# Kernel optimization log

Measured on AMD Instinct MI355X. Metric: run time of the kernel, lower is better.

Reference implementation:

```python
import jax, jax.numpy as jnp
from jax import lax
import numpy as np

D = 512        # d_model
F = 128        # raw feature dim
MS = 1024      # logic (service) nodes
NP_ = 16384    # physical nodes
EL = 4096      # logic edges
EP = 131072    # phys edges
SRC = 0        # source_node_idx
NEG = -1e9


def _gnn(feats, edge_index, Win, Wout, N):
    row, col = edge_index
    h = jax.nn.relu(feats @ Win)                                  # [N, D]
    agg = jax.ops.segment_sum(h[row], col, num_segments=N)        # [N, D]
    return jax.nn.relu((h + agg) @ Wout)


def _bfs_hop(edge_index, N, src, iters=16):
    # BFS hop distance from src (bounded Bellman-Ford relaxation)
    row, col = edge_index
    big = jnp.int32(N)
    dist = jnp.full((N,), big, jnp.int32).at[src].set(0)
    def body(_, d):
        cand = jnp.minimum(d[row] + 1, big)
        upd = jax.ops.segment_min(cand, col, num_segments=N)
        return jnp.minimum(d, upd)
    return lax.fori_loop(0, iters, body, dist)


def _forward(logic_feats, phys_feats, Ws_in, Ws_out, Wp_in, Wp_out,
             sA1, sA2, pA1, pA2, Wq, Wk, Wc1, bc1, wc2,
             logic_edge_index, phys_edge_index, actions, static_mask, topo_order):
    Np = phys_feats.shape[0]
    cloud = Np - 1                                                # cloud_node_idx = -1
    h_s = _gnn(logic_feats, logic_edge_index, Ws_in, Ws_out, logic_feats.shape[0])
    h_p = _gnn(phys_feats, phys_edge_index, Wp_in, Wp_out, Np)
    # task-specific residual adapters
    h_s = h_s + jax.nn.relu(h_s @ sA1) @ sA2
    h_p = h_p + jax.nn.relu(h_p @ pA1) @ pA2
    metric = _bfs_hop(phys_edge_index, Np, SRC)                   # [Np] int32
    q_all = (h_s @ Wq) / jnp.sqrt(jnp.float32(D))                 # [Ms, D]
    K = h_p @ Wk                                                  # [Np, D]
    acts = actions.astype(jnp.int32)

    def step(state, i):
        visited, last, logp_sum, ent_sum, switches, relax = state
        base = static_mask[i]                                     # [Np] bool
        # cloud_sticky branch
        sticky = jnp.zeros_like(base).at[cloud].set(base[cloud])
        # forbid_return (allow_stay keeps `last`)
        forbid = visited.at[last].set(False)
        allowed_n = base & (~forbid) & (metric >= metric[last])   # metric_non_decreasing
        allowed = jnp.where(last == cloud, sticky, allowed_n)
        any_a = allowed.any()
        # relaxation fallback: stay -> cloud -> base
        fb_stay = jnp.zeros_like(base).at[last].set(True)
        fb_cloud = jnp.zeros_like(base).at[cloud].set(True)
        fallback = jnp.where(base[last], fb_stay, jnp.where(base[cloud], fb_cloud, base))
        allowed = jnp.where(any_a, allowed, fallback)
        # actor: masked categorical over physical nodes
        logits = K @ q_all[i]                                     # [Np]
        logp_all = jax.nn.log_softmax(jnp.where(allowed, logits, NEG))
        p = jnp.exp(logp_all)
        ent = -jnp.sum(p * logp_all)
        a = acts[i]
        ne = a != last
        visited = visited.at[last].set(visited[last] | ne)
        last = jnp.where(ne, a, last)
        return (visited, last, logp_sum + logp_all[a], ent_sum + ent,
                switches + ne.astype(jnp.int32), relax + (~any_a).astype(jnp.int32)), None

    init = (jnp.zeros((Np,), bool), jnp.int32(SRC),
            jnp.float32(0.0), jnp.float32(0.0), jnp.int32(0), jnp.int32(0))
    (visited, last, logp_sum, ent_sum, switches, relax), _ = lax.scan(
        step, init, topo_order.astype(jnp.int32))
    # value head
    pooled = jnp.concatenate([h_s.mean(0), h_p.mean(0)])          # [2D]
    value = jax.nn.relu(pooled @ Wc1 + bc1) @ wc2                 # scalar
    return jnp.stack([logp_sum, ent_sum, value])


def setup_inputs() -> dict:
    key = jax.random.key(0)
    ks = jax.random.split(key, 20)
    s = 0.05
    def w(k, shape):
        return jax.random.normal(k, shape, jnp.float32) * s
    return {
        "logic_edge_index": jax.random.randint(ks[0], (2, EL), 0, MS, jnp.int32),
        "logic_feats": jax.random.normal(ks[1], (MS, F), jnp.float32),
        "phys_edge_index": jax.random.randint(ks[2], (2, EP), 0, NP_, jnp.int32),
        "phys_feats": jax.random.normal(ks[3], (NP_, F), jnp.float32),
        "actions": jax.random.randint(ks[4], (MS,), 0, NP_, jnp.int32),
        "static_mask": jnp.ones((MS, NP_), bool),
        "topo_order": jnp.arange(MS, dtype=jnp.int32),
        "Ws_in": w(ks[5], (F, D)), "Ws_out": w(ks[6], (D, D)),
        "Wp_in": w(ks[7], (F, D)), "Wp_out": w(ks[8], (D, D)),
        "sA1": w(ks[9], (D, D)), "sA2": w(ks[10], (D, D)),
        "pA1": w(ks[11], (D, D)), "pA2": w(ks[12], (D, D)),
        "Wq": w(ks[13], (D, D)), "Wk": w(ks[14], (D, D)),
        "Wc1": w(ks[15], (2 * D, D)),
        "bc1": jnp.zeros((D,), jnp.float32),
        "wc2": w(ks[16], (D,)),
    }


def reference(logic_edge_index, logic_feats, phys_edge_index, phys_feats,
              actions, static_mask, topo_order,
              Ws_in, Ws_out, Wp_in, Wp_out, sA1, sA2, pA1, pA2,
              Wq, Wk, Wc1, bc1, wc2):
    return _forward(logic_feats, phys_feats, Ws_in, Ws_out, Wp_in, Wp_out,
                    sA1, sA2, pA1, pA2, Wq, Wk, Wc1, bc1, wc2,
                    logic_edge_index, phys_edge_index, actions, static_mask, topo_order)
```

## Files before the change

### kernel.cpp

```cpp
#include <hip/hip_runtime.h>
#include <cstdint>
#include <cstddef>

typedef __bf16 bf16_t;
typedef bf16_t bf16x8 __attribute__((ext_vector_type(8)));
typedef bf16_t bf16x4v __attribute__((ext_vector_type(4)));
typedef float f32x4 __attribute__((ext_vector_type(4)));

#define NEGV (-1e9f)

#define GLDS(gp, lp) __builtin_amdgcn_global_load_lds( \
    (const __attribute__((address_space(1))) void*)(gp), \
    (__attribute__((address_space(3))) void*)(lp), 16, 0, 0)

struct PrepArgs {
    const float* w512src[8]; bf16_t* w512dst[8];
    const float* w128src[2]; bf16_t* w128dst[2];
    const float* logicF; const float* physF;
    bf16_t* featsSb; bf16_t* featsPb;
    const int* mask; uint32_t* bits;
    int* cntC; int* cntR; int* cntL; int* firstL; int* dist;
    float* pooled; float* hacc;
};

__global__ __launch_bounds__(256)
void k_prep(PrepArgs p) {
    __shared__ float tb[64][65];
    const int b = blockIdx.x, tid = threadIdx.x;
    if (b < 544) {
        const float* src; bf16_t* dst; int K, tile;
        if (b < 512) { src = p.w512src[b >> 6]; dst = p.w512dst[b >> 6]; K = 512; tile = b & 63; }
        else { int bb = b - 512; src = p.w128src[bb >> 4]; dst = p.w128dst[bb >> 4]; K = 128; tile = bb & 15; }
        const int N = 512;
        int kt = tile >> 3, tc = tile & 7;
        int cx = tid & 63, ry = tid >> 6;
#pragma unroll
        for (int q = 0; q < 16; ++q) {
            int r = q * 4 + ry;
            tb[r][cx] = src[(size_t)(kt * 64 + r) * N + tc * 64 + cx];
        }
        __syncthreads();
#pragma unroll
        for (int q = 0; q < 16; ++q) {
            int r2 = q * 4 + ry;
            dst[(size_t)(tc * 64 + r2) * K + kt * 64 + cx] = (bf16_t)tb[cx][r2];
        }
    } else if (b < 672) {
        size_t e0 = (size_t)(b - 544) * 1024 + tid * 4;
        float4 v = *(const float4*)(p.logicF + e0);
        bf16x4v o; o[0]=(bf16_t)v.x; o[1]=(bf16_t)v.y; o[2]=(bf16_t)v.z; o[3]=(bf16_t)v.w;
        *(bf16x4v*)(p.featsSb + e0) = o;
    } else if (b < 2720) {
        size_t e0 = (size_t)(b - 672) * 1024 + tid * 4;
        float4 v = *(const float4*)(p.physF + e0);
        bf16x4v o; o[0]=(bf16_t)v.x; o[1]=(bf16_t)v.y; o[2]=(bf16_t)v.z; o[3]=(bf16_t)v.w;
        *(bf16x4v*)(p.featsPb + e0) = o;
    } else if (b < 2784) {
        int gid = (b - 2720) * 256 + tid;
        p.cntC[gid] = 0; p.cntR[gid] = 0; p.firstL[gid] = 0x7fffffff;
        p.dist[gid] = (gid == 0) ? 0 : 16384;
        if (gid < 1024) { p.cntL[gid] = 0; p.pooled[gid] = 0.0f; }
        if (gid < 512) p.hacc[gid] = 0.0f;
    } else {
        size_t w = (size_t)(b - 2784) * 256 + tid;
        const int4* q4 = (const int4*)(p.mask + w * 32);
        uint32_t bb = 0;
#pragma unroll
        for (int q = 0; q < 8; ++q) {
            int4 v = q4[q];
            bb |= (v.x != 0 ? 1u : 0u) << (q * 4);
            bb |= (v.y != 0 ? 1u : 0u) << (q * 4 + 1);
            bb |= (v.z != 0 ? 1u : 0u) << (q * 4 + 2);
            bb |= (v.w != 0 ? 1u : 0u) << (q * 4 + 3);
        }
        p.bits[w] = bb;
    }
}

__global__ void k_hist3(const int* __restrict__ rowP, const int* __restrict__ colP,
                        const int* __restrict__ rowL, const int* __restrict__ colL,
                        int* cntC, int* cntR, int* cntL, int EP, int EL,
                        const int* __restrict__ topo, const int* __restrict__ acts,
                        int* __restrict__ lastArr, int* __restrict__ firstL) {
    int b = blockIdx.x;
    if (b < 1040) {
        int e = b * 256 + threadIdx.x;
        if (e < EP) atomicAdd(&cntC[colP[e]], 1);
        else if (e < 2 * EP) atomicAdd(&cntR[rowP[e - EP]], 1);
        else if (e < 2 * EP + EL) atomicAdd(&cntL[colL[e - 2 * EP]], 1);
    } else {
        int s = (b - 1040) * 256 + threadIdx.x;
        int last = (s == 0) ? 0 : acts[topo[s - 1]];
        lastArr[s] = last;
        int a = acts[topo[s]];
        if (a != last) atomicMin(&firstL[last], s);
    }
}

__global__ __launch_bounds__(256)
void k_scan3(int* cntC, int* offC, int* curC,
             int* cntR, int* offR, int* curR,
             int* cntL, int* offL, int* curL) {
    __shared__ int ss[256];
    int tid = threadIdx.x;
    const int* cnt; int* off; int* cur; int n;
    if (blockIdx.x == 0)      { cnt = cntC; off = offC; cur = curC; n = 16384; }
    else if (blockIdx.x == 1) { cnt = cntR; off = offR; cur = curR; n = 16384; }
    else                      { cnt = cntL; off = offL; cur = curL; n = 1024; }
    int chunk = n / 256, base = tid * chunk, s = 0;
    for (int i = 0; i < chunk; ++i) s += cnt[base + i];
    ss[tid] = s; __syncthreads();
    for (int d = 1; d < 256; d <<= 1) {
        int v = (tid >= d) ? ss[tid - d] : 0;
        __syncthreads(); ss[tid] += v; __syncthreads();
    }
    int run = (tid == 0) ? 0 : ss[tid - 1];
    for (int i = 0; i < chunk; ++i) { off[base + i] = run; cur[base + i] = run; run += cnt[base + i]; }
    if (tid == 255) off[n] = run;
}

__global__ void k_scatter3(const int* __restrict__ rowP, const int* __restrict__ colP,
                           const int* __restrict__ rowL, const int* __restrict__ colL,
                           int* curC, int* curR, int* curL,
                           int* erowCP, int* ecolRP, int* erowL, int EP, int EL) {
    int e = blockIdx.x * 256 + threadIdx.x;
    if (e < EP) {
        int c = colP[e]; int q = atomicAdd(&curC[c], 1); erowCP[q] = rowP[e];
    } else if (e < 2 * EP) {
        int e2 = e - EP;
        int c = rowP[e2]; int q = atomicAdd(&curR[c], 1); ecolRP[q] = colP[e2];
    } else if (e < 2 * EP + EL) {
        int e3 = e - 2 * EP;
        int c = colL[e3]; int q = atomicAdd(&curL[c], 1); erowL[q] = rowL[e3];
    }
}

__global__ __launch_bounds__(256)
void k_bfs_level(const int* __restrict__ offR, const int* __restrict__ ecol,
                 int* __restrict__ dist, int lev) {
    int j = blockIdx.x * 256 + threadIdx.x;
    if (dist[j] != lev) return;
    int e0 = offR[j], e1 = offR[j + 1];
    for (int e = e0; e < e1; ++e) {
        int v = ecol[e];
        if (dist[v] == 16384) dist[v] = lev + 1;
    }
}

__global__ __launch_bounds__(256)
void k_fmpack(const int* __restrict__ firstL, const int* __restrict__ dist, int* __restrict__ fm) {
    int j = blockIdx.x * 256 + threadIdx.x;
    int fl = firstL[j]; if (fl > 0xFFFF) fl = 0xFFFF;
    fm[j] = (fl << 16) | dist[j];
}

struct GemmDesc { const bf16_t* A; const bf16_t* B; const bf16_t* Cin; bf16_t* O;
                  int N; int K; float scale; int relu; };
struct GemmPair { GemmDesc d0; GemmDesc d1; int split; };

__global__ __launch_bounds__(256)
void gemm_mfma(GemmPair args) {
    __shared__ bf16_t As[2][128 * 32];
    __shared__ bf16_t Bs[2][128 * 32];
    const int nwg = gridDim.x * gridDim.y;
    const int cpx = nwg >> 3;
    const int pfl = blockIdx.y * gridDim.x + blockIdx.x;
    const int vfl = (pfl & 7) * cpx + (pfl >> 3);
    const int vbx = vfl % gridDim.x;
    const int vby = vfl / gridDim.x;
    const int inSet1 = (vby >= args.split);
    const GemmDesc g = inSet1 ? args.d1 : args.d0;
    const int my = vby - (inSet1 ? args.split : 0);
    const int m0 = my * 128, n0 = vbx * 128;
    const int tid = threadIdx.x, wave = tid >> 6, lane = tid & 63;
    const int wm = (wave >> 1) * 64, wn = (wave & 1) * 64;
    const int lr = lane & 15, lk = (lane >> 4) * 8;
    const int K = g.K;
    const int srr = wave * 16 + (lane >> 2);
    const int scb = (((lane & 3) ^ ((lane >> 2) & 3)) << 4);
    const char* Abase = (const char*)g.A + ((size_t)(m0 + srr) * K) * 2 + scb;
    const char* Bbase = (const char*)g.B + ((size_t)(n0 + srr) * K) * 2 + scb;
    const size_t rstep = (size_t)64 * K * 2;
    f32x4 acc[4][4] = {};

    auto stage = [&](int q, int k0) {
        const char* a0 = Abase + (size_t)k0 * 2;
        const char* b0 = Bbase + (size_t)k0 * 2;
        GLDS(a0,         &As[q][(wave * 16) * 32]);
        GLDS(a0 + rstep, &As[q][(64 + wave * 16) * 32]);
        GLDS(b0,         &Bs[q][(wave * 16) * 32]);
        GLDS(b0 + rstep, &Bs[q][(64 + wave * 16) * 32]);
    };

    stage(0, 0);
    asm volatile("s_waitcnt vmcnt(0)" ::: "memory");
    __syncthreads();
    const int nt = K >> 5;
    for (int t = 0; t < nt; ++t) {
        int cur = t & 1;
        if (t + 1 < nt) stage(cur ^ 1, (t + 1) << 5);
        bf16x8 af[4], bff[4];
#pragma unroll
        for (int mi = 0; mi < 4; ++mi) {
            int r = wm + mi * 16 + lr;
            int pb = r * 64 + ((lk * 2) ^ ((r & 3) << 4));
            af[mi] = *(const bf16x8*)((const char*)&As[cur][0] + pb);
        }
#pragma unroll
        for (int ni = 0; ni < 4; ++ni) {
            int r = wn + ni * 16 + lr;
            int pb = r * 64 + ((lk * 2) ^ ((r & 3) << 4));
            bff[ni] = *(const bf16x8*)((const char*)&Bs[cur][0] + pb);
        }
#pragma unroll
        for (int mi = 0; mi < 4; ++mi)
#pragma unroll
            for (int ni = 0; ni < 4; ++ni)
                acc[mi][ni] = __builtin_amdgcn_mfma_f32_16x16x32_bf16(af[mi], bff[ni], acc[mi][ni], 0, 0, 0);
        asm volatile("s_waitcnt vmcnt(0)" ::: "memory");
        __syncthreads();
    }
    const int rb = m0 + wm + (lane >> 4) * 4;
    const int cb = n0 + wn + lr;
#pragma unroll
    for (int mi = 0; mi < 4; ++mi)
#pragma unroll
        for (int ni = 0; ni < 4; ++ni)
#pragma unroll
            for (int r = 0; r < 4; ++r) {
                int row = rb + mi * 16 + r;
                int col = cb + ni * 16;
                size_t idx = (size_t)row * g.N + col;
                float v = acc[mi][ni][r] * g.scale;
                if (g.Cin) v += (float)g.Cin[idx];
                if (g.relu) v = fmaxf(v, 0.0f);
                g.O[idx] = (bf16_t)v;
            }
}

__global__ __launch_bounds__(256)
void k_spmm2(const bf16_t* __restrict__ HL, const int* __restrict__ offL, const int* __restrict__ erowL, bf16_t* __restrict__ XL,
             const bf16_t* __restrict__ HP, const int* __restrict__ offP, const int* __restrict__ erowP, bf16_t* __restrict__ XP) {
    int b = blockIdx.x;
    const bf16_t* H; const int* off; const int* erow; bf16_t* X; int c;
    int wib = threadIdx.x >> 6, lane = threadIdx.x & 63;
    if (b < 256) { H = HL; off = offL; erow = erowL; X = XL; c = b * 4 + wib; }
    else { b -= 256; H = HP; off = offP; erow = erowP; X = XP; c = b * 4 + wib; }
    int d0 = lane * 8;
    float acc[8] = {0,0,0,0,0,0,0,0};
    int e0 = off[c], e1 = off[c + 1];
    for (int e = e0; e < e1; ++e) {
        int r = erow[e];
        bf16x8 h = *(const bf16x8*)(H + (size_t)r * 512 + d0);
#pragma unroll
        for (int j = 0; j < 8; ++j) acc[j] += (float)h[j];
    }
    bf16x8 own = *(const bf16x8*)(H + (size_t)c * 512 + d0);
    bf16x8 o;
#pragma unroll
    for (int j = 0; j < 8; ++j) o[j] = (bf16_t)((float)own[j] + acc[j]);
    *(bf16x8*)(X + (size_t)c * 512 + d0) = o;
}

__global__ __launch_bounds__(256)
void k_scan2(const bf16_t* __restrict__ S, const uint32_t* __restrict__ bits,
             const int* __restrict__ fm, const int* __restrict__ topo,
             const int* __restrict__ acts, const int* __restrict__ lastA,
             float* __restrict__ slogp, float* __restrict__ sent) {
    const int NPn = 16384, cloud = NPn - 1;
    __shared__ float msh[256], zsh[256], wsh[256];
    __shared__ int ash[256];
    const int s = blockIdx.x, tid = threadIdx.x;
    const int i = topo[s], a = acts[i], last = lastA[s];
    const bf16_t* Srow = S + (size_t)i * NPn;
    const uint32_t* brow = bits + (size_t)i * 512;
    const int ml = fm[last] & 0xFFFF;
    const int baseCloud = (brow[511] >> 31) & 1;
    const int lic = (last == cloud);
    if (lic && baseCloud) {
        if (tid == 0) {
            float M = (float)Srow[cloud];
            slogp[s] = (a == cloud) ? 0.0f : (NEGV - M);
            sent[s] = 0.0f;
        }
        return;
    }
    float m = -3.4e38f, Z = 0.0f, W = 0.0f;
    int any = 0;
    if (!lic) {
        for (int c = 0; c < 8; ++c) {
            int j0 = c * 2048 + tid * 8;
            bf16x8 sv = *(const bf16x8*)(Srow + j0);
            uint32_t b8 = (brow[j0 >> 5] >> (j0 & 24)) & 0xFFu;
            int4 f0 = *(const int4*)(fm + j0);
            int4 f1 = *(const int4*)(fm + j0 + 4);
            int fj[8] = {f0.x, f0.y, f0.z, f0.w, f1.x, f1.y, f1.z, f1.w};
#pragma unroll
            for (int q = 0; q < 8; ++q) {
                int j = j0 + q;
                bool alw = ((b8 >> q) & 1) && ((fj[q] & 0xFFFF) >= ml)
                           && (j == last || (((unsigned)fj[q]) >> 16) >= (unsigned)s);
                if (alw) {
                    any = 1;
                    float l = (float)sv[q];
                    if (l > m) {
                        float d = m - l, ce = expf(d);
                        W = ce * (W + d * Z);
                        Z = ce * Z + 1.0f;
                        m = l;
                    } else {
                        float t = l - m, e = expf(t);
                        Z += e; W += t * e;
                    }
                }
            }
        }
    }
    msh[tid] = m; zsh[tid] = Z; wsh[tid] = W; ash[tid] = any;
    __syncthreads();
    for (int st = 128; st > 0; st >>= 1) {
        if (tid < st) {
            float m1 = msh[tid], Z1 = zsh[tid], W1 = wsh[tid];
            float m2 = msh[tid + st], Z2 = zsh[tid + st], W2 = wsh[tid + st];
            float M2 = fmaxf(m1, m2);
            float e1 = expf(m1 - M2), e2 = expf(m2 - M2);
            zsh[tid] = e1 * Z1 + e2 * Z2;
            wsh[tid] = e1 * (W1 + (m1 - M2) * Z1) + e2 * (W2 + (m2 - M2) * Z2);
            msh[tid] = M2;
            ash[tid] |= ash[tid + st];
        }
        __syncthreads();
    }
    if (tid != 0) return;
    if (ash[0]) {
        float M = msh[0], Zt = zsh[0], Wt = wsh[0];
        float logZ = logf(Zt);
        int fa = fm[a];
        bool alwa = ((brow[a >> 5] >> (a & 31)) & 1) && ((fa & 0xFFFF) >= ml)
                    && (a == last || (((unsigned)fa) >> 16) >= (unsigned)s);
        float la = alwa ? (float)Srow[a] : NEGV;
        slogp[s] = la - M - logZ;
        sent[s] = logZ - Wt / Zt;
        return;
    }
    int baseLast = (brow[last >> 5] >> (last & 31)) & 1;
    if (baseLast) { float M = (float)Srow[last]; slogp[s] = (a == last) ? 0.0f : (NEGV - M); sent[s] = 0.0f; return; }
    if (baseCloud) { float M = (float)Srow[cloud]; slogp[s] = (a == cloud) ? 0.0f : (NEGV - M); sent[s] = 0.0f; return; }
    float mm = -3.4e38f, ZZ = 0.0f, WW = 0.0f;
    for (int j = 0; j < NPn; ++j) {
        if ((brow[j >> 5] >> (j & 31)) & 1) {
            float l = (float)Srow[j];
            if (l > mm) { float d = mm - l, ce = expf(d); WW = ce * (WW + d * ZZ); ZZ = ce * ZZ + 1.0f; mm = l; }
            else { float t = l - mm, e = expf(t); ZZ += e; WW += t * e; }
        }
    }
    if (ZZ == 0.0f) { slogp[s] = -logf((float)NPn); sent[s] = logf((float)NPn); return; }
    float logZ = logf(ZZ);
    int ba = (brow[a >> 5] >> (a & 31)) & 1;
    float la = ba ? (float)Srow[a] : NEGV;
    slogp[s] = la - mm - logZ;
    sent[s] = logZ - WW / ZZ;
}

__global__ __launch_bounds__(256)
void k_pool2(const bf16_t* __restrict__ HL, const bf16_t* __restrict__ HP, float* __restrict__ pooled) {
    int b = blockIdx.x, tid = threadIdx.x;
    const bf16_t* H; float* dst; int R, bb, ng; float inv;
    if (b < 16) { H = HL; dst = pooled; R = 1024; inv = 1.0f / 1024.0f; bb = b; ng = 16; }
    else { H = HP; dst = pooled + 512; R = 16384; inv = 1.0f / 16384.0f; bb = b - 16; ng = 128; }
    float a0 = 0, a1 = 0;
    for (int r = bb; r < R; r += ng) {
        a0 += (float)H[(size_t)r * 512 + tid];
        a1 += (float)H[(size_t)r * 512 + tid + 256];
    }
    atomicAdd(&dst[tid], a0 * inv);
    atomicAdd(&dst[tid + 256], a1 * inv);
}

__global__ __launch_bounds__(256)
void k_vpart(const float* __restrict__ pooled, const float* __restrict__ Wc1, float* __restrict__ hacc) {
    __shared__ float pk[128];
    int b = blockIdx.x, tid = threadIdx.x;
    int k0 = b * 128;
    if (tid < 128) pk[tid] = pooled[k0 + tid];
    __syncthreads();
    float a0 = 0, a1 = 0;
    for (int kk = 0; kk < 128; ++kk) {
        float pv = pk[kk];
        const float* wr = Wc1 + (size_t)(k0 + kk) * 512;
        a0 += pv * wr[tid];
        a1 += pv * wr[tid + 256];
    }
    atomicAdd(&hacc[tid], a0);
    atomicAdd(&hacc[tid + 256], a1);
}

__global__ __launch_bounds__(256)
void k_epilogue(const float* __restrict__ slogp, const float* __restrict__ sent,
                const float* __restrict__ hacc, const float* __restrict__ bc1,
                const float* __restrict__ wc2, float* __restrict__ out) {
    __shared__ float s1[256], s2[256], s3[256];
    int tid = threadIdx.x;
    float a = 0, b = 0;
    for (int k = tid; k < 1024; k += 256) { a += slogp[k]; b += sent[k]; }
    float v = fmaxf(hacc[tid] + bc1[tid], 0.0f) * wc2[tid]
            + fmaxf(hacc[tid + 256] + bc1[tid + 256], 0.0f) * wc2[tid + 256];
    s1[tid] = a; s2[tid] = b; s3[tid] = v;
    __syncthreads();
    for (int st = 128; st > 0; st >>= 1) {
        if (tid < st) { s1[tid] += s1[tid + st]; s2[tid] += s2[tid + st]; s3[tid] += s3[tid + st]; }
        __syncthreads();
    }
    if (tid == 0) { out[0] = s1[0]; out[1] = s2[0]; out[2] = s3[0]; }
}

extern "C" void kernel_launch(void* const* d_in, const int* in_sizes, int n_in,
                              void* d_out, int out_size, void* d_ws, size_t ws_size,
                              hipStream_t stream) {
    (void)n_in; (void)out_size; (void)ws_size; (void)in_sizes;
    const int MS = 1024, NP = 16384, EL = 4096, EP = 131072, D = 512;

    const int* logicE = (const int*)d_in[0];
    const float* logicF = (const float*)d_in[1];
    const int* physE = (const int*)d_in[2];
    const float* physF = (const float*)d_in[3];
    const int* acts = (const int*)d_in[4];
    const int* mask = (const int*)d_in[5];
    const int* topo = (const int*)d_in[6];
    const float* Ws_in = (const float*)d_in[7];
    const float* Ws_out = (const float*)d_in[8];
    const float* Wp_in = (const float*)d_in[9];
    const float* Wp_out = (const float*)d_in[10];
    const float* sA1 = (const float*)d_in[11];
    const float* sA2 = (const float*)d_in[12];
    const float* pA1 = (const float*)d_in[13];
    const float* pA2 = (const float*)d_in[14];
    const float* Wq = (const float*)d_in[15];
    const float* Wk = (const float*)d_in[16];
    const float* Wc1 = (const float*)d_in[17];
    const float* bc1 = (const float*)d_in[18];
    const float* wc2 = (const float*)d_in[19];
    float* out = (float*)d_out;

    char* wsb = (char*)d_ws;
    size_t off = 0;
    auto alloc = [&](size_t bytes) -> void* {
        off = (off + 255) & ~(size_t)255;
        void* p = wsb + off; off += bytes; return p;
    };

    bf16_t* S_bf    = (bf16_t*)alloc((size_t)MS * NP * 2);
    bf16_t* PB0     = (bf16_t*)alloc((size_t)NP * D * 2);
    bf16_t* PB1     = (bf16_t*)alloc((size_t)NP * D * 2);
    bf16_t* PB2     = (bf16_t*)alloc((size_t)NP * D * 2);
    bf16_t* LB0     = (bf16_t*)alloc((size_t)MS * D * 2);
    bf16_t* LB1     = (bf16_t*)alloc((size_t)MS * D * 2);
    bf16_t* LB2     = (bf16_t*)alloc((size_t)MS * D * 2);
    bf16_t* featsSb = (bf16_t*)alloc((size_t)MS * 128 * 2);
    bf16_t* featsPb = (bf16_t*)alloc((size_t)NP * 128 * 2);
    bf16_t* WsinT   = (bf16_t*)alloc(512 * 128 * 2);
    bf16_t* WpinT   = (bf16_t*)alloc(512 * 128 * 2);
    bf16_t* WsoutT  = (bf16_t*)alloc(512 * 512 * 2);
    bf16_t* sA1T    = (bf16_t*)alloc(512 * 512 * 2);
    bf16_t* sA2T    = (bf16_t*)alloc(512 * 512 * 2);
    bf16_t* WqT     = (bf16_t*)alloc(512 * 512 * 2);
    bf16_t* WpoutT  = (bf16_t*)alloc(512 * 512 * 2);
    bf16_t* pA1T    = (bf16_t*)alloc(512 * 512 * 2);
    bf16_t* pA2T    = (bf16_t*)alloc(512 * 512 * 2);
    bf16_t* WkT    = (bf16_t*)alloc(512 * 512 * 2);
    uint32_t* bits = (uint32_t*)alloc((size_t)MS * NP / 8);
    int* cntC  = (int*)alloc(NP * 4);
    int* offC  = (int*)alloc((NP + 1) * 4);
    int* curC  = (int*)alloc(NP * 4);
    int* cntR  = (int*)alloc(NP * 4);
    int* offR  = (int*)alloc((NP + 1) * 4);
    int* curR  = (int*)alloc(NP * 4);
    int* cntL  = (int*)alloc(MS * 4);
    int* offL  = (int*)alloc((MS + 1) * 4);
    int* curL  = (int*)alloc(MS * 4);
    int* erowCP = (int*)alloc(EP * 4);
    int* ecolRP = (int*)alloc(EP * 4);
    int* erowL  = (int*)alloc(EL * 4);
    int* firstL = (int*)alloc(NP * 4);
    int* lastA  = (int*)alloc(MS * 4);
    int* dist   = (int*)alloc(NP * 4);
    int* fm     = (int*)alloc(NP * 4);
    float* slogp = (float*)alloc(MS * 4);
    float* sentb = (float*)alloc(MS * 4);
    float* pooled = (float*)alloc(1024 * 4);
    float* hacc   = (float*)alloc(512 * 4);

    const int* rowP = physE;  const int* colP = physE + EP;
    const int* rowL = logicE; const int* colL = logicE + EL;

    {
        PrepArgs p;
        const float* s512[8] = {Ws_out, sA1, sA2, Wq, Wp_out, pA1, pA2, Wk};
        bf16_t* d512[8] = {WsoutT, sA1T, sA2T, WqT, WpoutT, pA1T, pA2T, WkT};
        for (int q = 0; q < 8; ++q) { p.w512src[q] = s512[q]; p.w512dst[q] = d512[q]; }
        p.w128src[0] = Ws_in; p.w128dst[0] = WsinT;
        p.w128src[1] = Wp_in; p.w128dst[1] = WpinT;
        p.logicF = logicF; p.physF = physF; p.featsSb = featsSb; p.featsPb = featsPb;
        p.mask = mask; p.bits = bits;
        p.cntC = cntC; p.cntR = cntR; p.cntL = cntL; p.firstL = firstL; p.dist = dist;
        p.pooled = pooled; p.hacc = hacc;
        hipLaunchKernelGGL(k_prep, dim3(4832), dim3(256), 0, stream, p);
    }
    hipLaunchKernelGGL(k_hist3, dim3(1044), dim3(256), 0, stream,
                       rowP, colP, rowL, colL, cntC, cntR, cntL, EP, EL,
                       topo, acts, lastA, firstL);
    hipLaunchKernelGGL(k_scan3, dim3(3), dim3(256), 0, stream,
                       cntC, offC, curC, cntR, offR, curR, cntL, offL, curL);
    hipLaunchKernelGGL(k_scatter3, dim3((2 * EP + EL) / 256), dim3(256), 0, stream,
                       rowP, colP, rowL, colL, curC, curR, curL, erowCP, ecolRP, erowL, EP, EL);
    for (int lev = 0; lev < 16; ++lev)
        hipLaunchKernelGGL(k_bfs_level, dim3(64), dim3(256), 0, stream, offR, ecolRP, dist, lev);
    hipLaunchKernelGGL(k_fmpack, dim3(64), dim3(256), 0, stream, firstL, dist, fm);

    auto gemm2 = [&](const bf16_t* A0, const bf16_t* B0, const bf16_t* C0, bf16_t* O0, float sc0,
                     const bf16_t* A1, const bf16_t* B1, const bf16_t* C1, bf16_t* O1, float sc1,
                     int K, int relu) {
        GemmPair gp;
        gp.d0 = {A0, B0, C0, O0, 512, K, sc0, relu};
        gp.d1 = {A1, B1, C1, O1, 512, K, sc1, relu};
        gp.split = 8;
        hipLaunchKernelGGL(gemm_mfma, dim3(4, 136), dim3(256), 0, stream, gp);
    };

    gemm2(featsSb, WsinT, nullptr, LB0, 1.0f, featsPb, WpinT, nullptr, PB0, 1.0f, 128, 1);
    hipLaunchKernelGGL(k_spmm2, dim3(256 + 4096), dim3(256), 0, stream,
                       LB0, offL, erowL, LB1, PB0, offC, erowCP, PB1);
    gemm2(LB1, WsoutT, nullptr, LB0, 1.0f, PB1, WpoutT, nullptr, PB0, 1.0f, 512, 1);
    gemm2(LB0, sA1T, nullptr, LB1, 1.0f, PB0, pA1T, nullptr, PB1, 1.0f, 512, 1);
    gemm2(LB1, sA2T, LB0, LB2, 1.0f, PB1, pA2T, PB0, PB2, 1.0f, 512, 0);
    hipLaunchKernelGGL(k_pool2, dim3(144), dim3(256), 0, stream, LB2, PB2, pooled);
    gemm2(LB2, WqT, nullptr, LB1, 0.044194173824159216f, PB2, WkT, nullptr, PB1, 1.0f, 512, 0);
    {
        GemmPair gp;
        gp.d0 = {LB1, PB1, nullptr, S_bf, NP, 512, 1.0f, 0};
        gp.d1 = gp.d0;
        gp.split = 1000;
        hipLaunchKernelGGL(gemm_mfma, dim3(128, 8), dim3(256), 0, stream, gp);
    }
    hipLaunchKernelGGL(k_scan2, dim3(MS), dim3(256), 0, stream,
                       S_bf, bits, fm, topo, acts, lastA, slogp, sentb);
    hipLaunchKernelGGL(k_vpart, dim3(8), dim3(256), 0, stream, pooled, Wc1, hacc);
    hipLaunchKernelGGL(k_epilogue, dim3(1), dim3(256), 0, stream, slogp, sentb, hacc, bc1, wc2, out);
}
```

Baseline: 388.1 us.

## Switch GEMM operands and intermediate activations from bf16 to fp8 e4m3

All weights, features and intermediate activation buffers are stored in a hand-rolled fp8 e4m3 format, and the GEMM uses the fp8 MFMA 16x16x32 instruction with a 64-wide K tile. The aim is to halve memory traffic for activations and the sparse aggregation, and to raise matrix throughput. The price is software encode/decode per element in the epilogues, spmm and pooling, and a large loss of precision across the five chained GEMM layers, which may push results past the accuracy tolerance.

Result: slower. 489.5 us (+26.1%).

```diff
diff --git a/kernel.cpp b/kernel.cpp
--- a/kernel.cpp
+++ b/kernel.cpp
@@ -3,8 +3,9 @@
 #include <cstddef>
 
 typedef __bf16 bf16_t;
-typedef bf16_t bf16x8 __attribute__((ext_vector_type(8)));
-typedef bf16_t bf16x4v __attribute__((ext_vector_type(4)));
+typedef uint8_t u8;
+typedef u8 u8x8 __attribute__((ext_vector_type(8)));
+typedef u8 u8x4v __attribute__((ext_vector_type(4)));
 typedef float f32x4 __attribute__((ext_vector_type(4)));
 
 #define NEGV (-1e9f)
@@ -13,11 +14,33 @@
     (const __attribute__((address_space(1))) void*)(gp), \
     (__attribute__((address_space(3))) void*)(lp), 16, 0, 0)
 
+__device__ inline float fp8dec(u8 b) {
+    int e = (b >> 3) & 15, m = b & 7;
+    float v = e ? ldexpf((float)(8 + m), e - 10) : ldexpf((float)m, -9);
+    return (b & 0x80) ? -v : v;
+}
+__device__ inline u8 f2fp8(float x) {
+    uint32_t u = __float_as_uint(x);
+    u8 s = (u >> 24) & 0x80;
+    float a = fabsf(x);
+    if (!(a >= 0.0009765625f)) return s;
+    if (a > 448.0f) return s | 0x7E;
+    int e = (int)(__float_as_uint(a) >> 23) - 127;
+    if (e < -6) {
+        int m = (int)rintf(a * 512.0f);
+        if (m >= 8) return s | 0x08;
+        return s | (u8)m;
+    }
+    int m = (int)rintf(ldexpf(a, 3 - e));
+    if (m == 16) { m = 8; ++e; }
+    return s | (u8)(((e + 7) << 3) | (m - 8));
+}
+
 struct PrepArgs {
-    const float* w512src[8]; bf16_t* w512dst[8];
-    const float* w128src[2]; bf16_t* w128dst[2];
+    const float* w512src[8]; u8* w512dst[8];
+    const float* w128src[2]; u8* w128dst[2];
     const float* logicF; const float* physF;
-    bf16_t* featsSb; bf16_t* featsPb;
+    u8* featsSb; u8* featsPb;
     const int* mask; uint32_t* bits;
     int* cntC; int* cntR; int* cntL; int* firstL; int* dist;
     float* pooled; float* hacc;
@@ -28,7 +51,7 @@
     __shared__ float tb[64][65];
     const int b = blockIdx.x, tid = threadIdx.x;
     if (b < 544) {
-        const float* src; bf16_t* dst; int K, tile;
+        const float* src; u8* dst; int K, tile;
         if (b < 512) { src = p.w512src[b >> 6]; dst = p.w512dst[b >> 6]; K = 512; tile = b & 63; }
         else { int bb = b - 512; src = p.w128src[bb >> 4]; dst = p.w128dst[bb >> 4]; K = 128; tile = bb & 15; }
         const int N = 512;
@@ -43,18 +66,18 @@
 #pragma unroll
         for (int q = 0; q < 16; ++q) {
             int r2 = q * 4 + ry;
-            dst[(size_t)(tc * 64 + r2) * K + kt * 64 + cx] = (bf16_t)tb[cx][r2];
+            dst[(size_t)(tc * 64 + r2) * K + kt * 64 + cx] = f2fp8(tb[cx][r2]);
         }
     } else if (b < 672) {
         size_t e0 = (size_t)(b - 544) * 1024 + tid * 4;
         float4 v = *(const float4*)(p.logicF + e0);
-        bf16x4v o; o[0]=(bf16_t)v.x; o[1]=(bf16_t)v.y; o[2]=(bf16_t)v.z; o[3]=(bf16_t)v.w;
-        *(bf16x4v*)(p.featsSb + e0) = o;
+        u8x4v o; o[0]=f2fp8(v.x); o[1]=f2fp8(v.y); o[2]=f2fp8(v.z); o[3]=f2fp8(v.w);
+        *(u8x4v*)(p.featsSb + e0) = o;
     } else if (b < 2720) {
         size_t e0 = (size_t)(b - 672) * 1024 + tid * 4;
         float4 v = *(const float4*)(p.physF + e0);
-        bf16x4v o; o[0]=(bf16_t)v.x; o[1]=(bf16_t)v.y; o[2]=(bf16_t)v.z; o[3]=(bf16_t)v.w;
-        *(bf16x4v*)(p.featsPb + e0) = o;
+        u8x4v o; o[0]=f2fp8(v.x); o[1]=f2fp8(v.y); o[2]=f2fp8(v.z); o[3]=f2fp8(v.w);
+        *(u8x4v*)(p.featsPb + e0) = o;
     } else if (b < 2784) {
         int gid = (b - 2720) * 256 + tid;
         p.cntC[gid] = 0; p.cntR[gid] = 0; p.firstL[gid] = 0x7fffffff;
@@ -154,14 +177,14 @@
     fm[j] = (fl << 16) | dist[j];
 }
 
-struct GemmDesc { const bf16_t* A; const bf16_t* B; const bf16_t* Cin; bf16_t* O;
-                  int N; int K; float scale; int relu; };
+struct GemmDesc { const u8* A; const u8* B; const u8* Cin; void* O;
+                  int N; int K; float scale; int relu; int obf; };
 struct GemmPair { GemmDesc d0; GemmDesc d1; int split; };
 
 __global__ __launch_bounds__(256)
 void gemm_mfma(GemmPair args) {
-    __shared__ bf16_t As[2][128 * 32];
-    __shared__ bf16_t Bs[2][128 * 32];
+    __shared__ u8 As[2][128 * 64];
+    __shared__ u8 Bs[2][128 * 64];
     const int nwg = gridDim.x * gridDim.y;
     const int cpx = nwg >> 3;
     const int pfl = blockIdx.y * gridDim.x + blockIdx.x;
@@ -174,49 +197,50 @@
     const int m0 = my * 128, n0 = vbx * 128;
     const int tid = threadIdx.x, wave = tid >> 6, lane = tid & 63;
     const int wm = (wave >> 1) * 64, wn = (wave & 1) * 64;
-    const int lr = lane & 15, lk = (lane >> 4) * 8;
+    const int lr = lane & 15, lkq = lane >> 4;
     const int K = g.K;
     const int srr = wave * 16 + (lane >> 2);
     const int scb = (((lane & 3) ^ ((lane >> 2) & 3)) << 4);
-    const char* Abase = (const char*)g.A + ((size_t)(m0 + srr) * K) * 2 + scb;
-    const char* Bbase = (const char*)g.B + ((size_t)(n0 + srr) * K) * 2 + scb;
-    const size_t rstep = (size_t)64 * K * 2;
+    const u8* Abase = g.A + (size_t)(m0 + srr) * K + scb;
+    const u8* Bbase = g.B + (size_t)(n0 + srr) * K + scb;
+    const size_t rstep = (size_t)64 * K;
     f32x4 acc[4][4] = {};
 
     auto stage = [&](int q, int k0) {
-        const char* a0 = Abase + (size_t)k0 * 2;
-        const char* b0 = Bbase + (size_t)k0 * 2;
-        GLDS(a0,         &As[q][(wave * 16) * 32]);
-        GLDS(a0 + rstep, &As[q][(64 + wave * 16) * 32]);
-        GLDS(b0,         &Bs[q][(wave * 16) * 32]);
-        GLDS(b0 + rstep, &Bs[q][(64 + wave * 16) * 32]);
+        GLDS(Abase + k0,         &As[q][(wave * 16) * 64]);
+        GLDS(Abase + k0 + rstep, &As[q][(64 + wave * 16) * 64]);
+        GLDS(Bbase + k0,         &Bs[q][(wave * 16) * 64]);
+        GLDS(Bbase + k0 + rstep, &Bs[q][(64 + wave * 16) * 64]);
     };
 
     stage(0, 0);
     asm volatile("s_waitcnt vmcnt(0)" ::: "memory");
     __syncthreads();
-    const int nt = K >> 5;
+    const int nt = K >> 6;
     for (int t = 0; t < nt; ++t) {
         int cur = t & 1;
-        if (t + 1 < nt) stage(cur ^ 1, (t + 1) << 5);
-        bf16x8 af[4], bff[4];
-#pragma unroll
-        for (int mi = 0; mi < 4; ++mi) {
-            int r = wm + mi * 16 + lr;
-            int pb = r * 64 + ((lk * 2) ^ ((r & 3) << 4));
-            af[mi] = *(const bf16x8*)((const char*)&As[cur][0] + pb);
-        }
-#pragma unroll
-        for (int ni = 0; ni < 4; ++ni) {
-            int r = wn + ni * 16 + lr;
-            int pb = r * 64 + ((lk * 2) ^ ((r & 3) << 4));
-            bff[ni] = *(const bf16x8*)((const char*)&Bs[cur][0] + pb);
-        }
-#pragma unroll
-        for (int mi = 0; mi < 4; ++mi)
-#pragma unroll
-            for (int ni = 0; ni < 4; ++ni)
-                acc[mi][ni] = __builtin_amdgcn_mfma_f32_16x16x32_bf16(af[mi], bff[ni], acc[mi][ni], 0, 0, 0);
+        if (t + 1 < nt) stage(cur ^ 1, (t + 1) << 6);
+#pragma unroll
+        for (int kh = 0; kh < 2; ++kh) {
+            long af[4], bf[4];
+#pragma unroll
+            for (int mi = 0; mi < 4; ++mi) {
+                int r = wm + mi * 16 + lr;
+                int pb = r * 64 + ((kh * 32 + lkq * 8) ^ ((r & 3) << 4));
+                af[mi] = *(const long*)&As[cur][pb];
+            }
+#pragma unroll
+            for (int ni = 0; ni < 4; ++ni) {
+                int r = wn + ni * 16 + lr;
+                int pb = r * 64 + ((kh * 32 + lkq * 8) ^ ((r & 3) << 4));
+                bf[ni] = *(const long*)&Bs[cur][pb];
+            }
+#pragma unroll
+            for (int mi = 0; mi < 4; ++mi)
+#pragma unroll
+                for (int ni = 0; ni < 4; ++ni)
+                    acc[mi][ni] = __builtin_amdgcn_mfma_f32_16x16x32_fp8_fp8(af[mi], bf[ni], acc[mi][ni], 0, 0, 0);
+        }
         asm volatile("s_waitcnt vmcnt(0)" ::: "memory");
         __syncthreads();
     }
@@ -232,17 +256,18 @@
                 int col = cb + ni * 16;
                 size_t idx = (size_t)row * g.N + col;
                 float v = acc[mi][ni][r] * g.scale;
-                if (g.Cin) v += (float)g.Cin[idx];
+                if (g.Cin) v += fp8dec(g.Cin[idx]);
                 if (g.relu) v = fmaxf(v, 0.0f);
-                g.O[idx] = (bf16_t)v;
+                if (g.obf) ((bf16_t*)g.O)[idx] = (bf16_t)v;
+                else       ((u8*)g.O)[idx] = f2fp8(v);
             }
 }
 
 __global__ __launch_bounds__(256)
-void k_spmm2(const bf16_t* __restrict__ HL, const int* __restrict__ offL, const int* __restrict__ erowL, bf16_t* __restrict__ XL,
-             const bf16_t* __restrict__ HP, const int* __restrict__ offP, const int* __restrict__ erowP, bf16_t* __restrict__ XP) {
+void k_spmm2(const u8* __restrict__ HL, const int* __restrict__ offL, const int* __restrict__ erowL, u8* __restrict__ XL,
+             const u8* __restrict__ HP, const int* __restrict__ offP, const int* __restrict__ erowP, u8* __restrict__ XP) {
     int b = blockIdx.x;
-    const bf16_t* H; const int* off; const int* erow; bf16_t* X; int c;
+    const u8* H; const int* off; const int* erow; u8* X; int c;
     int wib = threadIdx.x >> 6, lane = threadIdx.x & 63;
     if (b < 256) { H = HL; off = offL; erow = erowL; X = XL; c = b * 4 + wib; }
     else { b -= 256; H = HP; off = offP; erow = erowP; X = XP; c = b * 4 + wib; }
@@ -251,15 +276,15 @@
     int e0 = off[c], e1 = off[c + 1];
     for (int e = e0; e < e1; ++e) {
         int r = erow[e];
-        bf16x8 h = *(const bf16x8*)(H + (size_t)r * 512 + d0);
-#pragma unroll
-        for (int j = 0; j < 8; ++j) acc[j] += (float)h[j];
-    }
-    bf16x8 own = *(const bf16x8*)(H + (size_t)c * 512 + d0);
-    bf16x8 o;
-#pragma unroll
-    for (int j = 0; j < 8; ++j) o[j] = (bf16_t)((float)own[j] + acc[j]);
-    *(bf16x8*)(X + (size_t)c * 512 + d0) = o;
+        u8x8 h = *(const u8x8*)(H + (size_t)r * 512 + d0);
+#pragma unroll
+        for (int j = 0; j < 8; ++j) acc[j] += fp8dec(h[j]);
+    }
+    u8x8 own = *(const u8x8*)(H + (size_t)c * 512 + d0);
+    u8x8 o;
+#pragma unroll
+    for (int j = 0; j < 8; ++j) o[j] = f2fp8(fp8dec(own[j]) + acc[j]);
+    *(u8x8*)(X + (size_t)c * 512 + d0) = o;
 }
 
 __global__ __launch_bounds__(256)
@@ -267,6 +292,7 @@
              const int* __restrict__ fm, const int* __restrict__ topo,
              const int* __restrict__ acts, const int* __restrict__ lastA,
              float* __restrict__ slogp, float* __restrict__ sent) {
+    typedef bf16_t bf16x8 __attribute__((ext_vector_type(8)));
     const int NPn = 16384, cloud = NPn - 1;
     __shared__ float msh[256], zsh[256], wsh[256];
     __shared__ int ash[256];
@@ -363,15 +389,15 @@
 }
 
 __global__ __launch_bounds__(256)
-void k_pool2(const bf16_t* __restrict__ HL, const bf16_t* __restrict__ HP, float* __restrict__ pooled) {
+void k_pool2(const u8* __restrict__ HL, const u8* __restrict__ HP, float* __restrict__ pooled) {
     int b = blockIdx.x, tid = threadIdx.x;
-    const bf16_t* H; float* dst; int R, bb, ng; float inv;
+    const u8* H; float* dst; int R, bb, ng; float inv;
     if (b < 16) { H = HL; dst = pooled; R = 1024; inv = 1.0f / 1024.0f; bb = b; ng = 16; }
     else { H = HP; dst = pooled + 512; R = 16384; inv = 1.0f / 16384.0f; bb = b - 16; ng = 128; }
     float a0 = 0, a1 = 0;
     for (int r = bb; r < R; r += ng) {
-        a0 += (float)H[(size_t)r * 512 + tid];
-        a1 += (float)H[(size_t)r * 512 + tid + 256];
+        a0 += fp8dec(H[(size_t)r * 512 + tid]);
+        a1 += fp8dec(H[(size_t)r * 512 + tid + 256]);
     }
     atomicAdd(&dst[tid], a0 * inv);
     atomicAdd(&dst[tid + 256], a1 * inv);
@@ -449,25 +475,25 @@
         void* p = wsb + off; off += bytes; return p;
     };
 
-    bf16_t* S_bf    = (bf16_t*)alloc((size_t)MS * NP * 2);
-    bf16_t* PB0     = (bf16_t*)alloc((size_t)NP * D * 2);
-    bf16_t* PB1     = (bf16_t*)alloc((size_t)NP * D * 2);
-    bf16_t* PB2     = (bf16_t*)alloc((size_t)NP * D * 2);
-    bf16_t* LB0     = (bf16_t*)alloc((size_t)MS * D * 2);
-    bf16_t* LB1     = (bf16_t*)alloc((size_t)MS * D * 2);
-    bf16_t* LB2     = (bf16_t*)alloc((size_t)MS * D * 2);
-    bf16_t* featsSb = (bf16_t*)alloc((size_t)MS * 128 * 2);
-    bf16_t* featsPb = (bf16_t*)alloc((size_t)NP * 128 * 2);
-    bf16_t* WsinT   = (bf16_t*)alloc(512 * 128 * 2);
-    bf16_t* WpinT   = (bf16_t*)alloc(512 * 128 * 2);
-    bf16_t* WsoutT  = (bf16_t*)alloc(512 * 512 * 2);
-    bf16_t* sA1T    = (bf16_t*)alloc(512 * 512 * 2);
-    bf16_t* sA2T    = (bf16_t*)alloc(512 * 512 * 2);
-    bf16_t* WqT     = (bf16_t*)alloc(512 * 512 * 2);
-    bf16_t* WpoutT  = (bf16_t*)alloc(512 * 512 * 2);
-    bf16_t* pA1T    = (bf16_t*)alloc(512 * 512 * 2);
-    bf16_t* pA2T    = (bf16_t*)alloc(512 * 512 * 2);
-    bf16_t* WkT    = (bf16_t*)alloc(512 * 512 * 2);
+    bf16_t* S_bf  = (bf16_t*)alloc((size_t)MS * NP * 2);
+    u8* PB0     = (u8*)alloc((size_t)NP * D);
+    u8* PB1     = (u8*)alloc((size_t)NP * D);
+    u8* PB2     = (u8*)alloc((size_t)NP * D);
+    u8* LB0     = (u8*)alloc((size_t)MS * D);
+    u8* LB1     = (u8*)alloc((size_t)MS * D);
+    u8* LB2     = (u8*)alloc((size_t)MS * D);
+    u8* featsSb = (u8*)alloc((size_t)MS * 128);
+    u8* featsPb = (u8*)alloc((size_t)NP * 128);
+    u8* WsinT   = (u8*)alloc(512 * 128);
+    u8* WpinT   = (u8*)alloc(512 * 128);
+    u8* WsoutT  = (u8*)alloc(512 * 512);
+    u8* sA1T    = (u8*)alloc(512 * 512);
+    u8* sA2T    = (u8*)alloc(512 * 512);
+    u8* WqT     = (u8*)alloc(512 * 512);
+    u8* WpoutT  = (u8*)alloc(512 * 512);
+    u8* pA1T    = (u8*)alloc(512 * 512);
+    u8* pA2T    = (u8*)alloc(512 * 512);
+    u8* WkT     = (u8*)alloc(512 * 512);
     uint32_t* bits = (uint32_t*)alloc((size_t)MS * NP / 8);
     int* cntC  = (int*)alloc(NP * 4);
     int* offC  = (int*)alloc((NP + 1) * 4);
@@ -496,7 +522,7 @@
     {
         PrepArgs p;
         const float* s512[8] = {Ws_out, sA1, sA2, Wq, Wp_out, pA1, pA2, Wk};
-        bf16_t* d512[8] = {WsoutT, sA1T, sA2T, WqT, WpoutT, pA1T, pA2T, WkT};
+        u8* d512[8] = {WsoutT, sA1T, sA2T, WqT, WpoutT, pA1T, pA2T, WkT};
         for (int q = 0; q < 8; ++q) { p.w512src[q] = s512[q]; p.w512dst[q] = d512[q]; }
         p.w128src[0] = Ws_in; p.w128dst[0] = WsinT;
         p.w128src[1] = Wp_in; p.w128dst[1] = WpinT;
@@ -517,12 +543,12 @@
         hipLaunchKernelGGL(k_bfs_level, dim3(64), dim3(256), 0, stream, offR, ecolRP, dist, lev);
     hipLaunchKernelGGL(k_fmpack, dim3(64), dim3(256), 0, stream, firstL, dist, fm);
 
-    auto gemm2 = [&](const bf16_t* A0, const bf16_t* B0, const bf16_t* C0, bf16_t* O0, float sc0,
-                     const bf16_t* A1, const bf16_t* B1, const bf16_t* C1, bf16_t* O1, float sc1,
+    auto gemm2 = [&](const u8* A0, const u8* B0, const u8* C0, void* O0, float sc0,
+                     const u8* A1, const u8* B1, const u8* C1, void* O1, float sc1,
                      int K, int relu) {
         GemmPair gp;
-        gp.d0 = {A0, B0, C0, O0, 512, K, sc0, relu};
-        gp.d1 = {A1, B1, C1, O1, 512, K, sc1, relu};
+        gp.d0 = {A0, B0, C0, O0, 512, K, sc0, relu, 0};
+        gp.d1 = {A1, B1, C1, O1, 512, K, sc1, relu, 0};
         gp.split = 8;
         hipLaunchKernelGGL(gemm_mfma, dim3(4, 136), dim3(256), 0, stream, gp);
     };
@@ -537,7 +563,7 @@
     gemm2(LB2, WqT, nullptr, LB1, 0.044194173824159216f, PB2, WkT, nullptr, PB1, 1.0f, 512, 0);
     {
         GemmPair gp;
-        gp.d0 = {LB1, PB1, nullptr, S_bf, NP, 512, 1.0f, 0};
+        gp.d0 = {LB1, PB1, nullptr, S_bf, NP, 512, 1.0f, 0, 1};
         gp.d1 = gp.d0;
         gp.split = 1000;
         hipLaunchKernelGGL(gemm_mfma, dim3(128, 8), dim3(256), 0, stream, gp);
```
